# Performance work log

Measured on AMD Instinct MI355X. Metric: run time of the kernel, lower is better.

The kernel has to match this reference:

```python
import jax, jax.numpy as jnp
import numpy as np

N_NODES = 100000
N_EDGES = 1600000
IN_FEATS, HIDDEN, OUT_MU, OUT_LV = 256, 128, 64, 64


def setup_inputs() -> dict:
    key = jax.random.key(0)
    ks = jax.random.split(key, 8)
    X = jax.random.normal(ks[0], (N_NODES, IN_FEATS), dtype=jnp.float32)
    edge_index = jax.random.randint(ks[1], (2, N_EDGES), 0, N_NODES, dtype=jnp.int64)
    def glorot(k, shape):
        lim = np.sqrt(6.0 / (shape[0] + shape[1])).astype(np.float32)
        return jax.random.uniform(k, shape, jnp.float32, -lim, lim)
    W1 = glorot(ks[2], (IN_FEATS, HIDDEN))
    b1 = jnp.zeros((HIDDEN,), jnp.float32)
    Wmu = glorot(ks[3], (HIDDEN, OUT_MU))
    bmu = jnp.zeros((OUT_MU,), jnp.float32)
    Wlv = glorot(ks[4], (HIDDEN, OUT_LV))
    blv = jnp.zeros((OUT_LV,), jnp.float32)
    return {"X": X, "edge_index": edge_index, "W1": W1, "b1": b1,
            "Wmu": Wmu, "bmu": bmu, "Wlv": Wlv, "blv": blv}


def _gcn_norm(edge_index, num_nodes):
    # Add self-loops (PyG GCNConv default) and compute symmetric normalization.
    loop = jnp.arange(num_nodes, dtype=edge_index.dtype)
    row = jnp.concatenate([edge_index[0], loop])  # source
    col = jnp.concatenate([edge_index[1], loop])  # target
    deg = jax.ops.segment_sum(jnp.ones_like(col, dtype=jnp.float32), col,
                              num_segments=num_nodes)
    dinv = jnp.where(deg > 0, jax.lax.rsqrt(deg), 0.0)
    norm = dinv[row] * dinv[col]  # [E+N]
    return row, col, norm


def _gcn_conv(x, W, b, row, col, norm, num_nodes):
    # Linear transform, then normalized sparse neighbor aggregation at targets.
    h = x @ W                                   # [N, F_out]
    msg = h[row] * norm[:, None]                # gather + scale, [E+N, F_out]
    out = jax.ops.segment_sum(msg, col, num_segments=num_nodes)
    return out + b


def reference(X, edge_index, W1, b1, Wmu, bmu, Wlv, blv):
    n = X.shape[0]
    row, col, norm = _gcn_norm(edge_index, n)
    H = jax.nn.relu(_gcn_conv(X, W1, b1, row, col, norm, n))
    mu = _gcn_conv(H, Wmu, bmu, row, col, norm, n)
    lv = _gcn_conv(H, Wlv, blv, row, col, norm, n)
    return (mu, lv)
```

## Files before the change

kernel.cpp:

```cpp
#include <hip/hip_runtime.h>
#include <hip/hip_bf16.h>
#include <cstdint>

#define N_FEATS_IN 256
#define HID 128
#define OUTF 64
#define SITEMS 8
#define NXCD 8
#define XS_STRIDE 264

typedef __bf16 bf16x8 __attribute__((ext_vector_type(8)));
typedef __bf16 bf16x4 __attribute__((ext_vector_type(4)));
typedef __bf16 bf16x2 __attribute__((ext_vector_type(2)));
typedef float f32x4 __attribute__((ext_vector_type(4)));

__device__ __forceinline__ int xcc_id() {
  int x;
  asm volatile("s_getreg_b32 %0, hwreg(HW_REG_XCC_ID, 0, 32)" : "=s"(x));
  return x & (NXCD - 1);
}


__global__ __launch_bounds__(256) void count_deg_kernel(const int* __restrict__ ei, int E,
    int N, int* __restrict__ cnt8, int* __restrict__ erank) {
  int e = blockIdx.x * 256 + threadIdx.x;
  int x = xcc_id();
  if (e < E) {
    int c = ei[E + e];
    int lr = __hip_atomic_fetch_add(&cnt8[(size_t)x * N + c], 1,
                                    __ATOMIC_RELAXED, __HIP_MEMORY_SCOPE_WORKGROUP);
    erank[e] = lr | (x << 28);
  }
}

__global__ __launch_bounds__(256) void combine_kernel(int* __restrict__ cnt8,
    int* __restrict__ deg, float* __restrict__ dinv, int n) {
  int c = blockIdx.x * 256 + threadIdx.x;
  if (c < n) {
    int s = 0;
#pragma unroll
    for (int x = 0; x < NXCD; ++x) {
      int v = cnt8[(size_t)x * n + c];
      cnt8[(size_t)x * n + c] = s;
      s += v;
    }
    deg[c] = s;
    dinv[c] = rsqrtf((float)(s + 1));
  }
}


__global__ __launch_bounds__(256) void scan_part_kernel(const int* __restrict__ cnt, int n,
                                                        int* __restrict__ bsum) {
  __shared__ int ts[256];
  const int t = threadIdx.x;
  int base = (blockIdx.x * 256 + t) * SITEMS;
  int s = 0;
#pragma unroll
  for (int i = 0; i < SITEMS; ++i) {
    int idx = base + i;
    if (idx < n) s += cnt[idx];
  }
  ts[t] = s;
  __syncthreads();
  for (int off = 128; off > 0; off >>= 1) {
    if (t < off) ts[t] += ts[t + off];
    __syncthreads();
  }
  if (t == 0) bsum[blockIdx.x] = ts[0];
}

__global__ __launch_bounds__(256) void scan_bsum_kernel(int* __restrict__ bsum, int nb) {
  __shared__ int ts[256];
  const int t = threadIdx.x;
  int v = (t < nb) ? bsum[t] : 0;
  ts[t] = v;
  __syncthreads();
  for (int off = 1; off < 256; off <<= 1) {
    int u = (t >= off) ? ts[t - off] : 0;
    __syncthreads();
    ts[t] += u;
    __syncthreads();
  }
  if (t < nb) bsum[t] = ts[t] - v;
}

__global__ __launch_bounds__(256) void scan_final_kernel(const int* __restrict__ cnt, int n,
    const int* __restrict__ bsum, int* __restrict__ ptr) {
  __shared__ int ts[256];
  const int t = threadIdx.x;
  int base = (blockIdx.x * 256 + t) * SITEMS;
  int loc[SITEMS];
  int s = 0;
#pragma unroll
  for (int i = 0; i < SITEMS; ++i) {
    int idx = base + i;
    loc[i] = (idx < n) ? cnt[idx] : 0;
    s += loc[i];
  }
  ts[t] = s;
  __syncthreads();
  for (int off = 1; off < 256; off <<= 1) {
    int u = (t >= off) ? ts[t - off] : 0;
    __syncthreads();
    ts[t] += u;
    __syncthreads();
  }
  int run = bsum[blockIdx.x] + ts[t] - s;
#pragma unroll
  for (int i = 0; i < SITEMS; ++i) {
    int idx = base + i;
    if (idx < n) ptr[idx] = run;
    run += loc[i];
  }
  if (base < n && base + SITEMS >= n) ptr[n] = run;
}

__global__ __launch_bounds__(256) void fill_kernel(const int* __restrict__ ei, int E, int N,
    const int* __restrict__ ptr, const int* __restrict__ offs, const int* __restrict__ erank,
    const float* __restrict__ dinv, int2* __restrict__ erec) {
  int e = blockIdx.x * 256 + threadIdx.x;
  if (e < E) {
    int r = ei[e];
    int c = ei[E + e];
    int er = erank[e];
    int x = er >> 28;
    int lr = er & 0x0FFFFFFF;
    int pos = ptr[c] + offs[(size_t)x * N + c] + lr;
    int2 rec;
    rec.x = r;
    rec.y = __float_as_int(dinv[r] * dinv[c]);
    erec[pos] = rec;
  }
}


__global__ __launch_bounds__(256) void pack_all_kernel(const float* __restrict__ W1,
    const float* __restrict__ Wmu, const float* __restrict__ Wlv,
    __bf16* __restrict__ W1p, __bf16* __restrict__ Wcp) {
  int idx = blockIdx.x * 256 + threadIdx.x;
  if (idx < 32768) {
    int j = idx & 7, l = (idx >> 3) & 63, t = (idx >> 9) & 7, s = idx >> 12;
    int k = s * 32 + (l >> 4) * 8 + j;
    int n = t * 16 + (l & 15);
    W1p[idx] = (__bf16)W1[k * HID + n];
  } else if (idx < 49152) {
    int i2 = idx - 32768;
    int j = i2 & 7, l = (i2 >> 3) & 63, t = (i2 >> 9) & 7, s = i2 >> 12;
    int k = s * 32 + (l >> 4) * 8 + j;
    int g = t * 16 + (l & 15);
    float v = (g < OUTF) ? Wmu[k * OUTF + g] : Wlv[k * OUTF + (g - OUTF)];
    Wcp[i2] = (__bf16)v;
  }
}


__global__ __launch_bounds__(256) void gemm1_mfma(const float* __restrict__ X,
    const __bf16* __restrict__ Wp, __bf16* __restrict__ Yb, int nrows) {
  __shared__ __bf16 xs[128 * XS_STRIDE];
  const int tid = threadIdx.x;
  const int rowbase = blockIdx.x * 128;

#pragma unroll
  for (int i = 0; i < 32; ++i) {
    int idx = i * 256 + tid;
    int row = idx >> 6;
    int cc = idx & 63;
    int gr = min(rowbase + row, nrows - 1);
    float4 v = ((const float4*)(X + (size_t)gr * N_FEATS_IN))[cc];
    bf16x4 b;
    b[0] = (__bf16)v.x; b[1] = (__bf16)v.y; b[2] = (__bf16)v.z; b[3] = (__bf16)v.w;
    *(bf16x4*)(xs + row * XS_STRIDE + cc * 4) = b;
  }
  __syncthreads();

  const int lane = tid & 63;
  const int wave = tid >> 6;
  const int lm = lane & 15;
  const int q = lane >> 4;
  const bf16x8* wp = (const bf16x8*)Wp;

  f32x4 acc[2][8];
#pragma unroll
  for (int m = 0; m < 2; ++m)
#pragma unroll
    for (int t = 0; t < 8; ++t) acc[m][t] = (f32x4)0.f;

#pragma unroll
  for (int s = 0; s < 8; ++s) {
    bf16x8 a0 = *(const bf16x8*)(xs + (wave * 32 + lm) * XS_STRIDE + s * 32 + q * 8);
    bf16x8 a1 = *(const bf16x8*)(xs + (wave * 32 + 16 + lm) * XS_STRIDE + s * 32 + q * 8);
#pragma unroll
    for (int t = 0; t < 8; ++t) {
      bf16x8 b = wp[(s * 8 + t) * 64 + lane];
      acc[0][t] = __builtin_amdgcn_mfma_f32_16x16x32_bf16(a0, b, acc[0][t], 0, 0, 0);
      acc[1][t] = __builtin_amdgcn_mfma_f32_16x16x32_bf16(a1, b, acc[1][t], 0, 0, 0);
    }
  }
#pragma unroll
  for (int m = 0; m < 2; ++m) {
    int rb = rowbase + wave * 32 + m * 16 + q * 4;
#pragma unroll
    for (int t = 0; t < 8; ++t) {
#pragma unroll
      for (int r2 = 0; r2 < 4; ++r2) {
        int row = rb + r2;
        if (row < nrows) Yb[(size_t)row * HID + t * 16 + lm] = (__bf16)acc[m][t][r2];
      }
    }
  }
}


__global__ __launch_bounds__(64) void agg_kernel(const __bf16* __restrict__ Fin,
    const int* __restrict__ ptr, const int2* __restrict__ erec,
    const float* __restrict__ dinv, const float* __restrict__ bias,
    __bf16* __restrict__ Fout, int do_relu) {
  const int c = blockIdx.x;
  const int t = threadIdx.x;
  const float d = dinv[c];
  bf16x2 sv = ((const bf16x2*)(Fin + (size_t)c * HID))[t];
  float ax = d * d * (float)sv[0];
  float ay = d * d * (float)sv[1];
  const int beg = ptr[c], end = ptr[c + 1];
  int e = beg;
  for (; e + 8 <= end; e += 8) {
    int2 p[8];
#pragma unroll
    for (int i = 0; i < 8; ++i) p[i] = erec[e + i];
    bf16x2 v[8];
#pragma unroll
    for (int i = 0; i < 8; ++i) v[i] = ((const bf16x2*)(Fin + (size_t)p[i].x * HID))[t];
#pragma unroll
    for (int i = 0; i < 8; ++i) {
      float nn = __int_as_float(p[i].y);
      ax = fmaf(nn, (float)v[i][0], ax);
      ay = fmaf(nn, (float)v[i][1], ay);
    }
  }
  for (; e + 4 <= end; e += 4) {
    int2 p0 = erec[e], p1 = erec[e + 1], p2 = erec[e + 2], p3 = erec[e + 3];
    bf16x2 v0 = ((const bf16x2*)(Fin + (size_t)p0.x * HID))[t];
    bf16x2 v1 = ((const bf16x2*)(Fin + (size_t)p1.x * HID))[t];
    bf16x2 v2 = ((const bf16x2*)(Fin + (size_t)p2.x * HID))[t];
    bf16x2 v3 = ((const bf16x2*)(Fin + (size_t)p3.x * HID))[t];
    float n0 = __int_as_float(p0.y), n1 = __int_as_float(p1.y);
    float n2 = __int_as_float(p2.y), n3 = __int_as_float(p3.y);
    ax = fmaf(n0, (float)v0[0], ax); ay = fmaf(n0, (float)v0[1], ay);
    ax = fmaf(n1, (float)v1[0], ax); ay = fmaf(n1, (float)v1[1], ay);
    ax = fmaf(n2, (float)v2[0], ax); ay = fmaf(n2, (float)v2[1], ay);
    ax = fmaf(n3, (float)v3[0], ax); ay = fmaf(n3, (float)v3[1], ay);
  }
  for (; e < end; ++e) {
    int2 p = erec[e];
    float nn = __int_as_float(p.y);
    bf16x2 v = ((const bf16x2*)(Fin + (size_t)p.x * HID))[t];
    ax = fmaf(nn, (float)v[0], ax);
    ay = fmaf(nn, (float)v[1], ay);
  }
  if (do_relu) {
    ax = fmaxf(ax + bias[2 * t], 0.f);
    ay = fmaxf(ay + bias[2 * t + 1], 0.f);
  }
  bf16x2 o;
  o[0] = (__bf16)ax;
  o[1] = (__bf16)ay;
  ((bf16x2*)(Fout + (size_t)c * HID))[t] = o;
}


__global__ __launch_bounds__(256) void gemm2_mfma(const __bf16* __restrict__ Gb,
    const __bf16* __restrict__ Wp, const float* __restrict__ bmu,
    const float* __restrict__ blv, float* __restrict__ out, int nrows, int ntiles) {
  __shared__ __bf16 bs[16384];
  const int tid = threadIdx.x;
  {
    const float4* s4 = (const float4*)Wp;
    float4* d4 = (float4*)bs;
#pragma unroll
    for (int i = 0; i < 8; ++i) d4[tid + 256 * i] = s4[tid + 256 * i];
  }
  __syncthreads();
  const int lane = tid & 63;
  const int wave = tid >> 6;
  const int lm = lane & 15;
  const int q = lane >> 4;
  const bf16x8* bsv = (const bf16x8*)bs;

  float bv[8];
  size_t obase[8];
#pragma unroll
  for (int t = 0; t < 8; ++t) {
    int col = t * 16 + lm;
    bv[t] = (col < OUTF) ? bmu[col] : blv[col - OUTF];
    obase[t] = (col < OUTF) ? (size_t)col : ((size_t)nrows * OUTF + (col - OUTF));
  }

  for (int tile = blockIdx.x; tile < ntiles; tile += gridDim.x) {
    const int row0 = tile * 64 + wave * 16;
    const int r = min(row0 + lm, nrows - 1);
    const bf16x8* gp = (const bf16x8*)(Gb + (size_t)r * HID);

    bf16x8 xa[4];
#pragma unroll
    for (int s = 0; s < 4; ++s) xa[s] = gp[s * 4 + q];

    f32x4 acc[8];
#pragma unroll
    for (int t = 0; t < 8; ++t) acc[t] = (f32x4)0.f;

#pragma unroll
    for (int s = 0; s < 4; ++s) {
#pragma unroll
      for (int t = 0; t < 8; ++t)
        acc[t] = __builtin_amdgcn_mfma_f32_16x16x32_bf16(xa[s], bsv[(s * 8 + t) * 64 + lane],
                                                         acc[t], 0, 0, 0);
    }
#pragma unroll
    for (int t = 0; t < 8; ++t) {
#pragma unroll
      for (int r2 = 0; r2 < 4; ++r2) {
        int row = row0 + q * 4 + r2;
        if (row < nrows) out[obase[t] + (size_t)row * OUTF] = acc[t][r2] + bv[t];
      }
    }
  }
}


extern "C" void kernel_launch(void* const* d_in, const int* in_sizes, int n_in,
                              void* d_out, int out_size, void* d_ws, size_t ws_size,
                              hipStream_t stream) {
  const float* X   = (const float*)d_in[0];
  const int*   ei  = (const int*)d_in[1];
  const float* W1  = (const float*)d_in[2];
  const float* b1  = (const float*)d_in[3];
  const float* Wmu = (const float*)d_in[4];
  const float* bmu = (const float*)d_in[5];
  const float* Wlv = (const float*)d_in[6];
  const float* blv = (const float*)d_in[7];
  float* out = (float*)d_out;

  const int N = in_sizes[0] / N_FEATS_IN;
  const int E = in_sizes[1] / 2;

  char* ws = (char*)d_ws;
  size_t off = 0;
  auto alloc = [&](size_t bytes) -> void* {
    void* p = ws + off;
    off += (bytes + 255) & ~(size_t)255;
    return p;
  };
  __bf16* Yb  = (__bf16*)alloc((size_t)N * HID * 2);
  __bf16* Hb  = (__bf16*)alloc((size_t)N * HID * 2);
  float* dinv = (float*)alloc((size_t)N * 4);
  int*   deg  = (int*)alloc((size_t)N * 4);
  int*   ptr  = (int*)alloc((size_t)(N + 1) * 4);
  int*   cnt8 = (int*)alloc((size_t)NXCD * N * 4);
  int*   erank = (int*)alloc((size_t)E * 4);
  int2*  erec = (int2*)alloc((size_t)E * 8);
  __bf16* W1p = (__bf16*)alloc(32768 * 2);
  __bf16* Wcp = (__bf16*)alloc(16384 * 2);
  int*   bsum = (int*)alloc(256 * 4);
  (void)ws_size; (void)n_in; (void)out_size;

  hipMemsetAsync(cnt8, 0, (size_t)NXCD * N * 4, stream);

  int ge = (E + 255) / 256;
  int gn = (N + 255) / 256;
  int nb = (N + 256 * SITEMS - 1) / (256 * SITEMS);
  count_deg_kernel<<<ge, 256, 0, stream>>>(ei, E, N, cnt8, erank);
  combine_kernel<<<gn, 256, 0, stream>>>(cnt8, deg, dinv, N);
  scan_part_kernel<<<nb, 256, 0, stream>>>(deg, N, bsum);
  scan_bsum_kernel<<<1, 256, 0, stream>>>(bsum, nb);
  scan_final_kernel<<<nb, 256, 0, stream>>>(deg, N, bsum, ptr);
  fill_kernel<<<ge, 256, 0, stream>>>(ei, E, N, ptr, cnt8, erank, dinv, erec);
  pack_all_kernel<<<192, 256, 0, stream>>>(W1, Wmu, Wlv, W1p, Wcp);

  int g1 = (N + 127) / 128;
  gemm1_mfma<<<g1, 256, 0, stream>>>(X, W1p, Yb, N);
  agg_kernel<<<N, 64, 0, stream>>>(Yb, ptr, erec, dinv, b1, Hb, 1);
  agg_kernel<<<N, 64, 0, stream>>>(Hb, ptr, erec, dinv, b1, Yb, 0);
  int ntiles2 = (N + 63) / 64;
  int g2 = ntiles2 < 768 ? ntiles2 : 768;
  gemm2_mfma<<<g2, 256, 0, stream>>>(Yb, Wcp, bmu, blv, out, N, ntiles2);
}
```

Before: 455.9 us.

## Build CSR via two-level bucket sort and compute edge norms on the fly

Replaces the per-XCD atomic degree counting, multi-pass scan and fill kernels with a two-level bucket sort. Edges are first scattered into 256-node buckets using LDS-local counters, then each bucket is sorted by target inside LDS to produce ptr, dinv and a source-only CSR array. The aggregation kernel now reads 4-byte source indices, gathers dinv[src] per edge and applies the target dinv once at the end, so edge records shrink from 8 to 4 bytes. In exchange each edge costs an extra random dinv load, and buckets larger than the LDS capacity fall back to a slower global-memory path.

```diff
diff --git a/kernel.cpp b/kernel.cpp
--- a/kernel.cpp
+++ b/kernel.cpp
@@ -5,8 +5,8 @@
 #define N_FEATS_IN 256
 #define HID 128
 #define OUTF 64
-#define SITEMS 8
-#define NXCD 8
+#define NBMAX 400
+#define BCAP 6144
 #define XS_STRIDE 264
 
 typedef __bf16 bf16x8 __attribute__((ext_vector_type(8)));
@@ -14,123 +14,108 @@
 typedef __bf16 bf16x2 __attribute__((ext_vector_type(2)));
 typedef float f32x4 __attribute__((ext_vector_type(4)));
 
-__device__ __forceinline__ int xcc_id() {
-  int x;
-  asm volatile("s_getreg_b32 %0, hwreg(HW_REG_XCC_ID, 0, 32)" : "=s"(x));
-  return x & (NXCD - 1);
-}
-
-
-__global__ __launch_bounds__(256) void count_deg_kernel(const int* __restrict__ ei, int E,
-    int N, int* __restrict__ cnt8, int* __restrict__ erank) {
-  int e = blockIdx.x * 256 + threadIdx.x;
-  int x = xcc_id();
-  if (e < E) {
-    int c = ei[E + e];
-    int lr = __hip_atomic_fetch_add(&cnt8[(size_t)x * N + c], 1,
-                                    __ATOMIC_RELAXED, __HIP_MEMORY_SCOPE_WORKGROUP);
-    erank[e] = lr | (x << 28);
-  }
-}
-
-__global__ __launch_bounds__(256) void combine_kernel(int* __restrict__ cnt8,
-    int* __restrict__ deg, float* __restrict__ dinv, int n) {
-  int c = blockIdx.x * 256 + threadIdx.x;
-  if (c < n) {
-    int s = 0;
-#pragma unroll
-    for (int x = 0; x < NXCD; ++x) {
-      int v = cnt8[(size_t)x * n + c];
-      cnt8[(size_t)x * n + c] = s;
-      s += v;
-    }
-    deg[c] = s;
-    dinv[c] = rsqrtf((float)(s + 1));
-  }
-}
-
-
-__global__ __launch_bounds__(256) void scan_part_kernel(const int* __restrict__ cnt, int n,
-                                                        int* __restrict__ bsum) {
-  __shared__ int ts[256];
+
+__global__ __launch_bounds__(256) void bucket_count(const int* __restrict__ ei, int E,
+    int CH, int NB, int* __restrict__ gbk, int* __restrict__ bbase) {
+  __shared__ int cnt[NBMAX];
+  const int t = threadIdx.x, blk = blockIdx.x;
+  for (int i = t; i < NB; i += 256) cnt[i] = 0;
+  __syncthreads();
+  int base = blk * CH, lim = min(base + CH, E);
+  for (int i = base + t; i < lim; i += 256) atomicAdd(&cnt[ei[E + i] >> 8], 1);
+  __syncthreads();
+  for (int i = t; i < NB; i += 256) {
+    int b = (i + blk) % NB;
+    int v = cnt[b];
+    bbase[(size_t)blk * NB + b] = (v > 0) ? atomicAdd(&gbk[b], v) : 0;
+  }
+}
+
+__global__ __launch_bounds__(512) void bucket_scan(const int* __restrict__ gbk,
+    int* __restrict__ gbkoff, int NB, int E) {
+  __shared__ int ts[512];
   const int t = threadIdx.x;
-  int base = (blockIdx.x * 256 + t) * SITEMS;
-  int s = 0;
-#pragma unroll
-  for (int i = 0; i < SITEMS; ++i) {
-    int idx = base + i;
-    if (idx < n) s += cnt[idx];
-  }
-  ts[t] = s;
-  __syncthreads();
-  for (int off = 128; off > 0; off >>= 1) {
-    if (t < off) ts[t] += ts[t + off];
-    __syncthreads();
-  }
-  if (t == 0) bsum[blockIdx.x] = ts[0];
-}
-
-__global__ __launch_bounds__(256) void scan_bsum_kernel(int* __restrict__ bsum, int nb) {
-  __shared__ int ts[256];
-  const int t = threadIdx.x;
-  int v = (t < nb) ? bsum[t] : 0;
+  int v = (t < NB) ? gbk[t] : 0;
   ts[t] = v;
   __syncthreads();
-  for (int off = 1; off < 256; off <<= 1) {
+  for (int off = 1; off < 512; off <<= 1) {
     int u = (t >= off) ? ts[t - off] : 0;
     __syncthreads();
     ts[t] += u;
     __syncthreads();
   }
-  if (t < nb) bsum[t] = ts[t] - v;
-}
-
-__global__ __launch_bounds__(256) void scan_final_kernel(const int* __restrict__ cnt, int n,
-    const int* __restrict__ bsum, int* __restrict__ ptr) {
-  __shared__ int ts[256];
-  const int t = threadIdx.x;
-  int base = (blockIdx.x * 256 + t) * SITEMS;
-  int loc[SITEMS];
-  int s = 0;
-#pragma unroll
-  for (int i = 0; i < SITEMS; ++i) {
-    int idx = base + i;
-    loc[i] = (idx < n) ? cnt[idx] : 0;
-    s += loc[i];
-  }
-  ts[t] = s;
+  if (t < NB) gbkoff[t] = ts[t] - v;
+  if (t == 0) gbkoff[NB] = E;
+}
+
+__global__ __launch_bounds__(256) void bucket_scatter(const int* __restrict__ ei, int E,
+    int CH, int NB, const int* __restrict__ gbkoff, const int* __restrict__ bbase,
+    int2* __restrict__ bucketed) {
+  __shared__ int cur[NBMAX];
+  const int t = threadIdx.x, blk = blockIdx.x;
+  for (int i = t; i < NB; i += 256)
+    cur[i] = gbkoff[i] + bbase[(size_t)blk * NB + i];
+  __syncthreads();
+  int base = blk * CH, lim = min(base + CH, E);
+  for (int i = base + t; i < lim; i += 256) {
+    int s = ei[i];
+    int c = ei[E + i];
+    int p = atomicAdd(&cur[c >> 8], 1);
+    bucketed[p] = make_int2(s, c);
+  }
+}
+
+__global__ __launch_bounds__(256) void bucket_csr(const int2* __restrict__ bucketed,
+    const int* __restrict__ gbkoff, int NB, int N, int E,
+    float* __restrict__ dinv, int* __restrict__ ptr, int* __restrict__ csrc) {
+  __shared__ int2 eb[BCAP];
+  __shared__ int cnt[256], scn[256], cur[256];
+  const int b = blockIdx.x, t = threadIdx.x;
+  const int beg = gbkoff[b], end = gbkoff[b + 1];
+  const int M = end - beg;
+  cnt[t] = 0;
+  __syncthreads();
+  const bool inlds = (M <= BCAP);
+  if (inlds) {
+    for (int i = t; i < M; i += 256) {
+      int2 r = bucketed[beg + i];
+      eb[i] = r;
+      atomicAdd(&cnt[r.y & 255], 1);
+    }
+  } else {
+    for (int i = t; i < M; i += 256) atomicAdd(&cnt[bucketed[beg + i].y & 255], 1);
+  }
+  __syncthreads();
+  const int c0 = cnt[t];
+  scn[t] = c0;
   __syncthreads();
   for (int off = 1; off < 256; off <<= 1) {
-    int u = (t >= off) ? ts[t - off] : 0;
+    int u = (t >= off) ? scn[t - off] : 0;
     __syncthreads();
-    ts[t] += u;
+    scn[t] += u;
     __syncthreads();
   }
-  int run = bsum[blockIdx.x] + ts[t] - s;
-#pragma unroll
-  for (int i = 0; i < SITEMS; ++i) {
-    int idx = base + i;
-    if (idx < n) ptr[idx] = run;
-    run += loc[i];
-  }
-  if (base < n && base + SITEMS >= n) ptr[n] = run;
-}
-
-__global__ __launch_bounds__(256) void fill_kernel(const int* __restrict__ ei, int E, int N,
-    const int* __restrict__ ptr, const int* __restrict__ offs, const int* __restrict__ erank,
-    const float* __restrict__ dinv, int2* __restrict__ erec) {
-  int e = blockIdx.x * 256 + threadIdx.x;
-  if (e < E) {
-    int r = ei[e];
-    int c = ei[E + e];
-    int er = erank[e];
-    int x = er >> 28;
-    int lr = er & 0x0FFFFFFF;
-    int pos = ptr[c] + offs[(size_t)x * N + c] + lr;
-    int2 rec;
-    rec.x = r;
-    rec.y = __float_as_int(dinv[r] * dinv[c]);
-    erec[pos] = rec;
+  const int excl = scn[t] - c0;
+  const int node = b * 256 + t;
+  if (node < N) {
+    ptr[node] = beg + excl;
+    dinv[node] = rsqrtf((float)(c0 + 1));
+  }
+  if (b == NB - 1 && t == 0) ptr[N] = E;
+  cur[t] = excl;
+  __syncthreads();
+  if (inlds) {
+    for (int i = t; i < M; i += 256) {
+      int2 r = eb[i];
+      int slot = atomicAdd(&cur[r.y & 255], 1);
+      csrc[beg + slot] = r.x;
+    }
+  } else {
+    for (int i = t; i < M; i += 256) {
+      int2 r = bucketed[beg + i];
+      int slot = atomicAdd(&cur[r.y & 255], 1);
+      csrc[beg + slot] = r.x;
+    }
   }
 }
 
@@ -213,51 +198,42 @@
 
 
 __global__ __launch_bounds__(64) void agg_kernel(const __bf16* __restrict__ Fin,
-    const int* __restrict__ ptr, const int2* __restrict__ erec,
+    const int* __restrict__ ptr, const int* __restrict__ csrc,
     const float* __restrict__ dinv, const float* __restrict__ bias,
     __bf16* __restrict__ Fout, int do_relu) {
   const int c = blockIdx.x;
   const int t = threadIdx.x;
   const float d = dinv[c];
   bf16x2 sv = ((const bf16x2*)(Fin + (size_t)c * HID))[t];
-  float ax = d * d * (float)sv[0];
-  float ay = d * d * (float)sv[1];
+  float ax = d * (float)sv[0];
+  float ay = d * (float)sv[1];
   const int beg = ptr[c], end = ptr[c + 1];
   int e = beg;
   for (; e + 8 <= end; e += 8) {
-    int2 p[8];
-#pragma unroll
-    for (int i = 0; i < 8; ++i) p[i] = erec[e + i];
+    int r[8];
+#pragma unroll
+    for (int i = 0; i < 8; ++i) r[i] = csrc[e + i];
+    float nr[8];
+#pragma unroll
+    for (int i = 0; i < 8; ++i) nr[i] = dinv[r[i]];
     bf16x2 v[8];
 #pragma unroll
-    for (int i = 0; i < 8; ++i) v[i] = ((const bf16x2*)(Fin + (size_t)p[i].x * HID))[t];
+    for (int i = 0; i < 8; ++i) v[i] = ((const bf16x2*)(Fin + (size_t)r[i] * HID))[t];
 #pragma unroll
     for (int i = 0; i < 8; ++i) {
-      float nn = __int_as_float(p[i].y);
-      ax = fmaf(nn, (float)v[i][0], ax);
-      ay = fmaf(nn, (float)v[i][1], ay);
-    }
-  }
-  for (; e + 4 <= end; e += 4) {
-    int2 p0 = erec[e], p1 = erec[e + 1], p2 = erec[e + 2], p3 = erec[e + 3];
-    bf16x2 v0 = ((const bf16x2*)(Fin + (size_t)p0.x * HID))[t];
-    bf16x2 v1 = ((const bf16x2*)(Fin + (size_t)p1.x * HID))[t];
-    bf16x2 v2 = ((const bf16x2*)(Fin + (size_t)p2.x * HID))[t];
-    bf16x2 v3 = ((const bf16x2*)(Fin + (size_t)p3.x * HID))[t];
-    float n0 = __int_as_float(p0.y), n1 = __int_as_float(p1.y);
-    float n2 = __int_as_float(p2.y), n3 = __int_as_float(p3.y);
-    ax = fmaf(n0, (float)v0[0], ax); ay = fmaf(n0, (float)v0[1], ay);
-    ax = fmaf(n1, (float)v1[0], ax); ay = fmaf(n1, (float)v1[1], ay);
-    ax = fmaf(n2, (float)v2[0], ax); ay = fmaf(n2, (float)v2[1], ay);
-    ax = fmaf(n3, (float)v3[0], ax); ay = fmaf(n3, (float)v3[1], ay);
+      ax = fmaf(nr[i], (float)v[i][0], ax);
+      ay = fmaf(nr[i], (float)v[i][1], ay);
+    }
   }
   for (; e < end; ++e) {
-    int2 p = erec[e];
-    float nn = __int_as_float(p.y);
-    bf16x2 v = ((const bf16x2*)(Fin + (size_t)p.x * HID))[t];
-    ax = fmaf(nn, (float)v[0], ax);
-    ay = fmaf(nn, (float)v[1], ay);
-  }
+    int r = csrc[e];
+    float nr = dinv[r];
+    bf16x2 v = ((const bf16x2*)(Fin + (size_t)r * HID))[t];
+    ax = fmaf(nr, (float)v[0], ax);
+    ay = fmaf(nr, (float)v[1], ay);
+  }
+  ax *= d;
+  ay *= d;
   if (do_relu) {
     ax = fmaxf(ax + bias[2 * t], 0.f);
     ay = fmaxf(ay + bias[2 * t + 1], 0.f);
@@ -351,36 +327,34 @@
     off += (bytes + 255) & ~(size_t)255;
     return p;
   };
-  __bf16* Yb  = (__bf16*)alloc((size_t)N * HID * 2);
-  __bf16* Hb  = (__bf16*)alloc((size_t)N * HID * 2);
-  float* dinv = (float*)alloc((size_t)N * 4);
-  int*   deg  = (int*)alloc((size_t)N * 4);
-  int*   ptr  = (int*)alloc((size_t)(N + 1) * 4);
-  int*   cnt8 = (int*)alloc((size_t)NXCD * N * 4);
-  int*   erank = (int*)alloc((size_t)E * 4);
-  int2*  erec = (int2*)alloc((size_t)E * 8);
-  __bf16* W1p = (__bf16*)alloc(32768 * 2);
-  __bf16* Wcp = (__bf16*)alloc(16384 * 2);
-  int*   bsum = (int*)alloc(256 * 4);
+  __bf16* Yb   = (__bf16*)alloc((size_t)N * HID * 2);
+  __bf16* Hb   = (__bf16*)alloc((size_t)N * HID * 2);
+  float* dinv  = (float*)alloc((size_t)N * 4);
+  int*   ptr   = (int*)alloc((size_t)(N + 1) * 4);
+  int2*  bucketed = (int2*)alloc((size_t)E * 8);
+  int*   csrc  = (int*)alloc((size_t)E * 4);
+  int*   gbk   = (int*)alloc((size_t)NBMAX * 4);
+  int*   gbkoff = (int*)alloc((size_t)(NBMAX + 1) * 4);
+  int*   bbase = (int*)alloc((size_t)256 * NBMAX * 4);
+  __bf16* W1p  = (__bf16*)alloc(32768 * 2);
+  __bf16* Wcp  = (__bf16*)alloc(16384 * 2);
   (void)ws_size; (void)n_in; (void)out_size;
 
-  hipMemsetAsync(cnt8, 0, (size_t)NXCD * N * 4, stream);
-
-  int ge = (E + 255) / 256;
-  int gn = (N + 255) / 256;
-  int nb = (N + 256 * SITEMS - 1) / (256 * SITEMS);
-  count_deg_kernel<<<ge, 256, 0, stream>>>(ei, E, N, cnt8, erank);
-  combine_kernel<<<gn, 256, 0, stream>>>(cnt8, deg, dinv, N);
-  scan_part_kernel<<<nb, 256, 0, stream>>>(deg, N, bsum);
-  scan_bsum_kernel<<<1, 256, 0, stream>>>(bsum, nb);
-  scan_final_kernel<<<nb, 256, 0, stream>>>(deg, N, bsum, ptr);
-  fill_kernel<<<ge, 256, 0, stream>>>(ei, E, N, ptr, cnt8, erank, dinv, erec);
+  const int NB = (N + 255) >> 8;
+  const int P = 256;
+  const int CH = (E + P - 1) / P;
+
+  hipMemsetAsync(gbk, 0, (size_t)NB * 4, stream);
+  bucket_count<<<P, 256, 0, stream>>>(ei, E, CH, NB, gbk, bbase);
+  bucket_scan<<<1, 512, 0, stream>>>(gbk, gbkoff, NB, E);
+  bucket_scatter<<<P, 256, 0, stream>>>(ei, E, CH, NB, gbkoff, bbase, bucketed);
+  bucket_csr<<<NB, 256, 0, stream>>>(bucketed, gbkoff, NB, N, E, dinv, ptr, csrc);
   pack_all_kernel<<<192, 256, 0, stream>>>(W1, Wmu, Wlv, W1p, Wcp);
 
   int g1 = (N + 127) / 128;
   gemm1_mfma<<<g1, 256, 0, stream>>>(X, W1p, Yb, N);
-  agg_kernel<<<N, 64, 0, stream>>>(Yb, ptr, erec, dinv, b1, Hb, 1);
-  agg_kernel<<<N, 64, 0, stream>>>(Hb, ptr, erec, dinv, b1, Yb, 0);
+  agg_kernel<<<N, 64, 0, stream>>>(Yb, ptr, csrc, dinv, b1, Hb, 1);
+  agg_kernel<<<N, 64, 0, stream>>>(Hb, ptr, csrc, dinv, b1, Yb, 0);
   int ntiles2 = (N + 63) / 64;
   int g2 = ntiles2 < 768 ? ntiles2 : 768;
   gemm2_mfma<<<g2, 256, 0, stream>>>(Yb, Wcp, bmu, blv, out, N, ntiles2);
```

New measurement: 402.5 us. -11.7%, faster.
